# Kernel tuning notes

Measured on AMD Instinct MI355X. Metric: run time of the kernel, lower is better.

The kernel has to match this reference:

```python
import jax, jax.numpy as jnp
import numpy as np

B, T, D_IN, H = 256, 512, 64, 128
S_MIN, S_FRAC = 0.5, 0.5


def _gru_cell(x_i, h, W_ih, W_hh, b_ih, b_hh):
    # torch.nn.GRUCell semantics
    gi = x_i @ W_ih.T + b_ih          # [B, 3H]
    gh = h @ W_hh.T + b_hh            # [B, 3H]
    i_r, i_z, i_n = jnp.split(gi, 3, axis=-1)
    h_r, h_z, h_n = jnp.split(gh, 3, axis=-1)
    r = jax.nn.sigmoid(i_r + h_r)
    z = jax.nn.sigmoid(i_z + h_z)
    n = jnp.tanh(i_n + r * h_n)
    return (1.0 - z) * n + z * h


def _rk4_step(h, dt, W_node, b_node):
    # one fixed RK4 step of dh/dt = tanh(h @ W_node^T + b_node) over [t, t+dt]
    f = lambda hh: jnp.tanh(hh @ W_node.T + b_node)
    k1 = f(h)
    k2 = f(h + 0.5 * dt * k1)
    k3 = f(h + 0.5 * dt * k2)
    k4 = f(h + dt * k3)
    return h + (dt / 6.0) * (k1 + 2.0 * k2 + 2.0 * k3 + k4)


def setup_inputs() -> dict:
    key = jax.random.key(0)
    ks = jax.random.split(key, 8)
    x = jax.random.normal(ks[0], (B, T, D_IN), dtype=jnp.float32)
    # sorted per-sample time grid; all lens == T so argmax-longest picks row 0
    tp = jnp.broadcast_to(jnp.linspace(0.01, 1.0, T, dtype=jnp.float32), (B, T))
    # generate_samp_mask(x, s_min=0.5, s_frac=0.5), deterministic seed
    rng = np.random.default_rng(0)
    minimum_ind = int(T * S_MIN)
    extrap_ind = int(rng.integers(minimum_ind, T))
    n_inds = int(S_FRAC * extrap_ind)
    samp_inds = np.sort(rng.choice(np.arange(extrap_ind), n_inds, replace=False))
    mask_np = np.zeros(T, dtype=bool)
    mask_np[samp_inds] = True
    samp_mask = jnp.asarray(mask_np)
    s = 1.0 / np.sqrt(H)
    W_ih = jax.random.uniform(ks[1], (3 * H, D_IN), jnp.float32, -s, s)
    W_hh = jax.random.uniform(ks[2], (3 * H, H), jnp.float32, -s, s)
    b_ih = jax.random.uniform(ks[3], (3 * H,), jnp.float32, -s, s)
    b_hh = jax.random.uniform(ks[4], (3 * H,), jnp.float32, -s, s)
    W_node = jax.random.normal(ks[5], (H, H), jnp.float32) * 0.05
    b_node = jnp.zeros((H,), jnp.float32)
    W_out = jax.random.uniform(ks[6], (D_IN, H), jnp.float32, -s, s)
    b_out = jax.random.uniform(ks[7], (D_IN,), jnp.float32, -s, s)
    return {"x": x, "tp": tp, "samp_mask": samp_mask,
            "W_ih": W_ih, "W_hh": W_hh, "b_ih": b_ih, "b_hh": b_hh,
            "W_node": W_node, "b_node": b_node, "W_out": W_out, "b_out": b_out}


def reference(x, tp, samp_mask, W_ih, W_hh, b_ih, b_hh, W_node, b_node, W_out, b_out):
    # get_longest_tp: all lens equal -> row 0; prepend tp[0]-0.01
    t0 = tp[0]                                   # [T]
    ts = jnp.concatenate([t0[:1] - 0.01, t0])    # [T+1]
    dts = ts[1:] - ts[:-1]                       # [T]
    xs = jnp.transpose(x, (1, 0, 2))             # [T, B, D_in]
    h0 = jnp.zeros((x.shape[0], W_hh.shape[1]), x.dtype)

    def step(h, inp):
        dt, x_i, use_x = inp
        h_ode = _rk4_step(h, dt, W_node, b_node)
        prev_out = h @ W_out.T + b_out           # teacher-forcing from own output
        inp_vec = jnp.where(use_x, x_i, prev_out)
        h_new = _gru_cell(inp_vec, h_ode, W_ih, W_hh, b_ih, b_hh)
        return h_new, h_new

    _, h_arr = jax.lax.scan(step, h0, (dts, xs, samp_mask))  # [T, B, H]
    h_arr = jnp.transpose(h_arr, (1, 0, 2))                  # [B, T, H]
    out = h_arr @ W_out.T + b_out                            # [B, T, D_in]
    # select_by_length with all lens == T -> flat [B*T, D_in]
    return out.reshape(-1, out.shape[-1])
```

## Files before the change

kernel.cpp:

```cpp
#include <hip/hip_runtime.h>


#define NB    256
#define TB    512
#define TSTEP 512
#define DIN   64
#define HD    128

typedef float v2f __attribute__((ext_vector_type(2)));

__device__ __forceinline__ float fast_tanh(float v) {
    float e = __expf(2.0f * v);
    return 1.0f - 2.0f / (e + 1.0f);
}
__device__ __forceinline__ float fast_sigmoid(float v) {
    return 1.0f / (1.0f + __expf(-v));
}

__device__ __forceinline__ float quad_red(float v) {
    v += __int_as_float(__builtin_amdgcn_update_dpp(
            0, __float_as_int(v), 0xB1, 0xF, 0xF, true));
    v += __int_as_float(__builtin_amdgcn_update_dpp(
            0, __float_as_int(v), 0x4E, 0xF, 0xF, true));
    return v;
}

__global__ __launch_bounds__(TB, 2) void gruode_kernel(
    const float* __restrict__ x,
    const float* __restrict__ tp,
    const int*   __restrict__ samp_mask,
    const float* __restrict__ W_ih,
    const float* __restrict__ W_hh,
    const float* __restrict__ b_ih,
    const float* __restrict__ b_hh,
    const float* __restrict__ W_node,
    const float* __restrict__ b_node,
    const float* __restrict__ W_out,
    const float* __restrict__ b_out,
    float*       __restrict__ out)
{
    const int t   = threadIdx.x;
    const int b   = blockIdx.x;
    const int j   = t >> 2;
    const int kq  = t & 3;
    const int j64 = t >> 3;
    const int ko  = t & 7;

    __shared__ __align__(16) float sh_h [HD];
    __shared__ __align__(16) float sh_t0[HD];
    __shared__ __align__(16) float sh_t1[HD];
    __shared__ __align__(16) float sh_in[DIN];
    __shared__ __align__(16) float sh_po[DIN];

    const float4* Wn4  = (const float4*)W_node;
    const float4* Whh4 = (const float4*)W_hh;
    const float4* Wih4 = (const float4*)W_ih;
    const float4* Wo4  = (const float4*)W_out;

    v2f Wn[16], Whr[16], Whz[16], Whn[16];
    #pragma unroll
    for (int i = 0; i < 8; ++i) {
        float4 w;
        w = Wn4 [j*32 + i*4 + kq];          Wn [2*i] = (v2f){w.x, w.y}; Wn [2*i+1] = (v2f){w.z, w.w};
        w = Whh4[(0*HD + j)*32 + i*4 + kq]; Whr[2*i] = (v2f){w.x, w.y}; Whr[2*i+1] = (v2f){w.z, w.w};
        w = Whh4[(1*HD + j)*32 + i*4 + kq]; Whz[2*i] = (v2f){w.x, w.y}; Whz[2*i+1] = (v2f){w.z, w.w};
        w = Whh4[(2*HD + j)*32 + i*4 + kq]; Whn[2*i] = (v2f){w.x, w.y}; Whn[2*i+1] = (v2f){w.z, w.w};
    }
    v2f Wir[8], Wiz[8], Win[8], Wo[8];
    #pragma unroll
    for (int i = 0; i < 4; ++i) {
        float4 w;
        w = Wih4[(0*HD + j)*16 + i*4 + kq]; Wir[2*i] = (v2f){w.x, w.y}; Wir[2*i+1] = (v2f){w.z, w.w};
        w = Wih4[(1*HD + j)*16 + i*4 + kq]; Wiz[2*i] = (v2f){w.x, w.y}; Wiz[2*i+1] = (v2f){w.z, w.w};
        w = Wih4[(2*HD + j)*16 + i*4 + kq]; Win[2*i] = (v2f){w.x, w.y}; Win[2*i+1] = (v2f){w.z, w.w};
        w = Wo4 [j64*32 + i*8 + ko];        Wo [2*i] = (v2f){w.x, w.y}; Wo [2*i+1] = (v2f){w.z, w.w};
    }
    #pragma unroll
    for (int i = 0; i < 16; ++i) {
        asm volatile("" : "+v"(Wn[i]));  asm volatile("" : "+v"(Whr[i]));
        asm volatile("" : "+v"(Whz[i])); asm volatile("" : "+v"(Whn[i]));
    }
    #pragma unroll
    for (int i = 0; i < 8; ++i) {
        asm volatile("" : "+v"(Wir[i])); asm volatile("" : "+v"(Wiz[i]));
        asm volatile("" : "+v"(Win[i])); asm volatile("" : "+v"(Wo[i]));
    }

    const float bn   = b_node[j];
    const float br   = b_ih[0*HD + j] + b_hh[0*HD + j];
    const float bz   = b_ih[1*HD + j] + b_hh[1*HD + j];
    const float bi_n = b_ih[2*HD + j];
    const float bh_n = b_hh[2*HD + j];
    const float bo   = b_out[j64];

    if (t < HD)  sh_h[t]  = 0.0f;
    if (t < DIN) sh_po[t] = b_out[t];

    float tp_cur  = tp[0];
    float tp_prev = tp_cur - 0.01f;
    int   m_cur   = samp_mask[0];
    float xr = (t < DIN) ? x[(size_t)b * TSTEP * DIN + t] : 0.0f;

    __syncthreads();

    const float4* h4  = (const float4*)sh_h;
    const float4* t04 = (const float4*)sh_t0;
    const float4* t14 = (const float4*)sh_t1;
    const float4* in4 = (const float4*)sh_in;

    auto hdot = [&](const v2f (&w)[16], const float4* buf) -> float {
        v2f a0 = {0.f, 0.f}, a1 = {0.f, 0.f};
        #pragma unroll
        for (int i = 0; i < 8; ++i) {
            float4 v = buf[i*4 + kq];
            a0 += w[2*i]   * (v2f){v.x, v.y};
            a1 += w[2*i+1] * (v2f){v.z, v.w};
        }
        v2f a = a0 + a1;
        return a.x + a.y;
    };

    float hj = 0.0f;

    #pragma unroll 1
    for (int s = 0; s < TSTEP; ++s) {
        const float dt = tp_cur - tp_prev;

        if (t < DIN) sh_in[t] = m_cur ? xr : sh_po[t];

        {
            const int sn = (s + 1 < TSTEP) ? s + 1 : s;
            tp_prev = tp_cur;
            tp_cur  = tp[sn];
            m_cur   = samp_mask[sn];
            if (t < DIN) xr = x[((size_t)b * TSTEP + sn) * DIN + t];
        }

        float k1 = fast_tanh(quad_red(hdot(Wn, h4)) + bn);
        if (kq == 0) sh_t0[j] = fmaf(0.5f * dt, k1, hj);
        __syncthreads();

        float k2 = fast_tanh(quad_red(hdot(Wn, t04)) + bn);
        if (kq == 0) sh_t1[j] = fmaf(0.5f * dt, k2, hj);
        __syncthreads();

        float k3 = fast_tanh(quad_red(hdot(Wn, t14)) + bn);
        if (kq == 0) sh_t0[j] = fmaf(dt, k3, hj);
        __syncthreads();

        float k4 = fast_tanh(quad_red(hdot(Wn, t04)) + bn);
        float hode = fmaf(dt * (1.0f / 6.0f),
                          (k1 + 2.0f * k2) + (2.0f * k3 + k4), hj);
        if (kq == 0) sh_t1[j] = hode;
        __syncthreads();

        v2f ar = {0.f,0.f}, az = {0.f,0.f}, an = {0.f,0.f};
        #pragma unroll
        for (int i = 0; i < 8; ++i) {
            float4 v = t14[i*4 + kq];
            v2f lo = {v.x, v.y}, hi = {v.z, v.w};
            ar += Whr[2*i] * lo; ar += Whr[2*i+1] * hi;
            az += Whz[2*i] * lo; az += Whz[2*i+1] * hi;
            an += Whn[2*i] * lo; an += Whn[2*i+1] * hi;
        }
        v2f cr = {0.f,0.f}, cz = {0.f,0.f}, cn = {0.f,0.f};
        #pragma unroll
        for (int i = 0; i < 4; ++i) {
            float4 v = in4[i*4 + kq];
            v2f lo = {v.x, v.y}, hi = {v.z, v.w};
            cr += Wir[2*i] * lo; cr += Wir[2*i+1] * hi;
            cz += Wiz[2*i] * lo; cz += Wiz[2*i+1] * hi;
            cn += Win[2*i] * lo; cn += Win[2*i+1] * hi;
        }
        float rr  = fast_sigmoid(quad_red((ar.x + ar.y) + (cr.x + cr.y)) + br);
        float zz  = fast_sigmoid(quad_red((az.x + az.y) + (cz.x + cz.y)) + bz);
        float hnv = quad_red(an.x + an.y) + bh_n;
        float inv = quad_red(cn.x + cn.y) + bi_n;
        float nn  = fast_tanh(fmaf(rr, hnv, inv));
        float hnew = fmaf(zz, hode - nn, nn);
        hj = hnew;

        if (kq == 0) sh_h[j] = hnew;
        __syncthreads();

        v2f ao = {0.f, 0.f};
        #pragma unroll
        for (int i = 0; i < 4; ++i) {
            float4 v = h4[i*8 + ko];
            ao += Wo[2*i]   * (v2f){v.x, v.y};
            ao += Wo[2*i+1] * (v2f){v.z, v.w};
        }
        float o = quad_red(ao.x + ao.y);
        o += __shfl_xor(o, 4);
        o += bo;
        if (ko == 0) {
            sh_po[j64] = o;
            out[((size_t)b * TSTEP + s) * DIN + j64] = o;
        }
        __syncthreads();
    }
}

extern "C" void kernel_launch(void* const* d_in, const int* in_sizes, int n_in,
                              void* d_out, int out_size, void* d_ws, size_t ws_size,
                              hipStream_t stream) {
    (void)in_sizes; (void)n_in; (void)d_ws; (void)ws_size; (void)out_size;
    const float* x      = (const float*)d_in[0];
    const float* tp     = (const float*)d_in[1];
    const int*   mask   = (const int*)  d_in[2];
    const float* W_ih   = (const float*)d_in[3];
    const float* W_hh   = (const float*)d_in[4];
    const float* b_ih   = (const float*)d_in[5];
    const float* b_hh   = (const float*)d_in[6];
    const float* W_node = (const float*)d_in[7];
    const float* b_node = (const float*)d_in[8];
    const float* W_out  = (const float*)d_in[9];
    const float* b_out  = (const float*)d_in[10];
    float* outp = (float*)d_out;

    gruode_kernel<<<NB, TB, 0, stream>>>(x, tp, mask, W_ih, W_hh, b_ih, b_hh,
                                         W_node, b_node, W_out, b_out, outp);
}
```

Baseline: 1.225 ms.

## Remap to 16-lane groups computing 4 rows each with DPP scan reductions

Each thread now owns a 16-wide slice of the K dimension for four output rows, rather than a quarter of one row. Per-row sums are reduced across the 16 lanes with row_shr DPP scans, and the total is broadcast with a quad_perm so each of the last four lanes picks up one row. The GRU input vector is now read directly from registers (x) or sh_po, which removes the sh_in staging buffer and one barrier per timestep, and x is loaded as float4. Fewer barriers and wider loads are traded for more DPP instructions per reduction and a select at the end of every dot product.

```diff
diff --git a/kernel.cpp b/kernel.cpp
--- a/kernel.cpp
+++ b/kernel.cpp
@@ -17,15 +17,25 @@
     return 1.0f / (1.0f + __expf(-v));
 }
 
-__device__ __forceinline__ float quad_red(float v) {
-    v += __int_as_float(__builtin_amdgcn_update_dpp(
-            0, __float_as_int(v), 0xB1, 0xF, 0xF, true));
-    v += __int_as_float(__builtin_amdgcn_update_dpp(
-            0, __float_as_int(v), 0x4E, 0xF, 0xF, true));
+template<int CTRL>
+__device__ __forceinline__ float dpp_add(float v) {
+    return v + __int_as_float(__builtin_amdgcn_update_dpp(
+        0, __float_as_int(v), CTRL, 0xF, 0xF, true));
+}
+__device__ __forceinline__ float scan16(float v) {
+    v = dpp_add<0x111>(v);
+    v = dpp_add<0x112>(v);
+    v = dpp_add<0x114>(v);
+    v = dpp_add<0x118>(v);
     return v;
 }
-
-__global__ __launch_bounds__(TB, 2) void gruode_kernel(
+__device__ __forceinline__ float qp3333(float v) {
+    return __int_as_float(__builtin_amdgcn_update_dpp(
+        0, __float_as_int(v), 0xFF, 0xF, 0xF, true));
+}
+
+__global__ __launch_bounds__(TB) __attribute__((amdgpu_waves_per_eu(2, 2)))
+void gruode_kernel(
     const float* __restrict__ x,
     const float* __restrict__ tp,
     const int*   __restrict__ samp_mask,
@@ -39,17 +49,15 @@
     const float* __restrict__ b_out,
     float*       __restrict__ out)
 {
-    const int t   = threadIdx.x;
-    const int b   = blockIdx.x;
-    const int j   = t >> 2;
-    const int kq  = t & 3;
-    const int j64 = t >> 3;
-    const int ko  = t & 7;
+    const int t    = threadIdx.x;
+    const int b    = blockIdx.x;
+    const int g    = t >> 4;
+    const int kk   = t & 15;
+    const int rsel = kk & 3;
 
     __shared__ __align__(16) float sh_h [HD];
     __shared__ __align__(16) float sh_t0[HD];
     __shared__ __align__(16) float sh_t1[HD];
-    __shared__ __align__(16) float sh_in[DIN];
     __shared__ __align__(16) float sh_po[DIN];
 
     const float4* Wn4  = (const float4*)W_node;
@@ -57,41 +65,57 @@
     const float4* Wih4 = (const float4*)W_ih;
     const float4* Wo4  = (const float4*)W_out;
 
-    v2f Wn[16], Whr[16], Whz[16], Whn[16];
-    #pragma unroll
-    for (int i = 0; i < 8; ++i) {
-        float4 w;
-        w = Wn4 [j*32 + i*4 + kq];          Wn [2*i] = (v2f){w.x, w.y}; Wn [2*i+1] = (v2f){w.z, w.w};
-        w = Whh4[(0*HD + j)*32 + i*4 + kq]; Whr[2*i] = (v2f){w.x, w.y}; Whr[2*i+1] = (v2f){w.z, w.w};
-        w = Whh4[(1*HD + j)*32 + i*4 + kq]; Whz[2*i] = (v2f){w.x, w.y}; Whz[2*i+1] = (v2f){w.z, w.w};
-        w = Whh4[(2*HD + j)*32 + i*4 + kq]; Whn[2*i] = (v2f){w.x, w.y}; Whn[2*i+1] = (v2f){w.z, w.w};
-    }
-    v2f Wir[8], Wiz[8], Win[8], Wo[8];
+    v2f Wn[4][4], Whr[4][4], Whz[4][4], Whn[4][4];
+    v2f Wir[4][2], Wiz[4][2], Win[4][2];
+    v2f Wo[2][4];
+    #pragma unroll
+    for (int r = 0; r < 4; ++r) {
+        const int row = 4*g + r;
+        float4 a, c;
+        a = Wn4[row*32 + 2*kk];  c = Wn4[row*32 + 2*kk + 1];
+        Wn[r][0]=(v2f){a.x,a.y}; Wn[r][1]=(v2f){a.z,a.w}; Wn[r][2]=(v2f){c.x,c.y}; Wn[r][3]=(v2f){c.z,c.w};
+        a = Whh4[(0*HD+row)*32 + 2*kk];  c = Whh4[(0*HD+row)*32 + 2*kk + 1];
+        Whr[r][0]=(v2f){a.x,a.y}; Whr[r][1]=(v2f){a.z,a.w}; Whr[r][2]=(v2f){c.x,c.y}; Whr[r][3]=(v2f){c.z,c.w};
+        a = Whh4[(1*HD+row)*32 + 2*kk];  c = Whh4[(1*HD+row)*32 + 2*kk + 1];
+        Whz[r][0]=(v2f){a.x,a.y}; Whz[r][1]=(v2f){a.z,a.w}; Whz[r][2]=(v2f){c.x,c.y}; Whz[r][3]=(v2f){c.z,c.w};
+        a = Whh4[(2*HD+row)*32 + 2*kk];  c = Whh4[(2*HD+row)*32 + 2*kk + 1];
+        Whn[r][0]=(v2f){a.x,a.y}; Whn[r][1]=(v2f){a.z,a.w}; Whn[r][2]=(v2f){c.x,c.y}; Whn[r][3]=(v2f){c.z,c.w};
+        a = Wih4[(0*HD+row)*16 + kk];
+        Wir[r][0]=(v2f){a.x,a.y}; Wir[r][1]=(v2f){a.z,a.w};
+        a = Wih4[(1*HD+row)*16 + kk];
+        Wiz[r][0]=(v2f){a.x,a.y}; Wiz[r][1]=(v2f){a.z,a.w};
+        a = Wih4[(2*HD+row)*16 + kk];
+        Win[r][0]=(v2f){a.x,a.y}; Win[r][1]=(v2f){a.z,a.w};
+    }
+    #pragma unroll
+    for (int r = 0; r < 2; ++r) {
+        const int row = 2*g + r;
+        float4 a = Wo4[row*32 + 2*kk], c = Wo4[row*32 + 2*kk + 1];
+        Wo[r][0]=(v2f){a.x,a.y}; Wo[r][1]=(v2f){a.z,a.w}; Wo[r][2]=(v2f){c.x,c.y}; Wo[r][3]=(v2f){c.z,c.w};
+    }
+    #pragma unroll
+    for (int r = 0; r < 4; ++r) {
+        #pragma unroll
+        for (int i = 0; i < 4; ++i) {
+            asm volatile("" : "+v"(Wn[r][i]));  asm volatile("" : "+v"(Whr[r][i]));
+            asm volatile("" : "+v"(Whz[r][i])); asm volatile("" : "+v"(Whn[r][i]));
+        }
+        asm volatile("" : "+v"(Wir[r][0])); asm volatile("" : "+v"(Wir[r][1]));
+        asm volatile("" : "+v"(Wiz[r][0])); asm volatile("" : "+v"(Wiz[r][1]));
+        asm volatile("" : "+v"(Win[r][0])); asm volatile("" : "+v"(Win[r][1]));
+    }
     #pragma unroll
     for (int i = 0; i < 4; ++i) {
-        float4 w;
-        w = Wih4[(0*HD + j)*16 + i*4 + kq]; Wir[2*i] = (v2f){w.x, w.y}; Wir[2*i+1] = (v2f){w.z, w.w};
-        w = Wih4[(1*HD + j)*16 + i*4 + kq]; Wiz[2*i] = (v2f){w.x, w.y}; Wiz[2*i+1] = (v2f){w.z, w.w};
-        w = Wih4[(2*HD + j)*16 + i*4 + kq]; Win[2*i] = (v2f){w.x, w.y}; Win[2*i+1] = (v2f){w.z, w.w};
-        w = Wo4 [j64*32 + i*8 + ko];        Wo [2*i] = (v2f){w.x, w.y}; Wo [2*i+1] = (v2f){w.z, w.w};
-    }
-    #pragma unroll
-    for (int i = 0; i < 16; ++i) {
-        asm volatile("" : "+v"(Wn[i]));  asm volatile("" : "+v"(Whr[i]));
-        asm volatile("" : "+v"(Whz[i])); asm volatile("" : "+v"(Whn[i]));
-    }
-    #pragma unroll
-    for (int i = 0; i < 8; ++i) {
-        asm volatile("" : "+v"(Wir[i])); asm volatile("" : "+v"(Wiz[i]));
-        asm volatile("" : "+v"(Win[i])); asm volatile("" : "+v"(Wo[i]));
-    }
-
-    const float bn   = b_node[j];
-    const float br   = b_ih[0*HD + j] + b_hh[0*HD + j];
-    const float bz   = b_ih[1*HD + j] + b_hh[1*HD + j];
-    const float bi_n = b_ih[2*HD + j];
-    const float bh_n = b_hh[2*HD + j];
-    const float bo   = b_out[j64];
+        asm volatile("" : "+v"(Wo[0][i])); asm volatile("" : "+v"(Wo[1][i]));
+    }
+
+    const int rl  = 4*g + rsel;
+    const float bn   = b_node[rl];
+    const float br   = b_ih[0*HD + rl] + b_hh[0*HD + rl];
+    const float bz   = b_ih[1*HD + rl] + b_hh[1*HD + rl];
+    const float bin  = b_ih[2*HD + rl];
+    const float bhn  = b_hh[2*HD + rl];
+    const float bo   = b_out[2*g + (rsel & 1)];
 
     if (t < HD)  sh_h[t]  = 0.0f;
     if (t < DIN) sh_po[t] = b_out[t];
@@ -99,25 +123,34 @@
     float tp_cur  = tp[0];
     float tp_prev = tp_cur - 0.01f;
     int   m_cur   = samp_mask[0];
-    float xr = (t < DIN) ? x[(size_t)b * TSTEP * DIN + t] : 0.0f;
+    const float4* x4 = (const float4*)x;
+    float4 xr = x4[(size_t)b * TSTEP * 16 + kk];
 
     __syncthreads();
 
     const float4* h4  = (const float4*)sh_h;
     const float4* t04 = (const float4*)sh_t0;
     const float4* t14 = (const float4*)sh_t1;
-    const float4* in4 = (const float4*)sh_in;
-
-    auto hdot = [&](const v2f (&w)[16], const float4* buf) -> float {
-        v2f a0 = {0.f, 0.f}, a1 = {0.f, 0.f};
+    const float4* po4 = (const float4*)sh_po;
+
+    auto dot128 = [&](const v2f (&w)[4][4], const float4* buf, float (&acc)[4]) {
+        float4 a = buf[2*kk], c = buf[2*kk + 1];
+        v2f x0 = {a.x, a.y}, x1 = {a.z, a.w}, x2 = {c.x, c.y}, x3 = {c.z, c.w};
         #pragma unroll
-        for (int i = 0; i < 8; ++i) {
-            float4 v = buf[i*4 + kq];
-            a0 += w[2*i]   * (v2f){v.x, v.y};
-            a1 += w[2*i+1] * (v2f){v.z, v.w};
-        }
-        v2f a = a0 + a1;
-        return a.x + a.y;
+        for (int r = 0; r < 4; ++r) {
+            v2f s = w[r][0] * x0;
+            s = w[r][1] * x1 + s;
+            s = w[r][2] * x2 + s;
+            s = w[r][3] * x3 + s;
+            acc[r] = s.x + s.y;
+        }
+    };
+    auto reduce4 = [&](const float (&acc)[4]) -> float {
+        float s0 = qp3333(scan16(acc[0]));
+        float s1 = qp3333(scan16(acc[1]));
+        float s2 = qp3333(scan16(acc[2]));
+        float s3 = qp3333(scan16(acc[3]));
+        return rsel == 0 ? s0 : rsel == 1 ? s1 : rsel == 2 ? s2 : s3;
     };
 
     float hj = 0.0f;
@@ -125,79 +158,99 @@
     #pragma unroll 1
     for (int s = 0; s < TSTEP; ++s) {
         const float dt = tp_cur - tp_prev;
-
-        if (t < DIN) sh_in[t] = m_cur ? xr : sh_po[t];
+        float acc[4], p, k1, k2, k3, k4;
+
+        dot128(Wn, h4, acc);
+        p  = reduce4(acc);
+        k1 = fast_tanh(p + bn);
+        if (kk >= 12) sh_t0[4*g + rsel] = fmaf(0.5f * dt, k1, hj);
+        __syncthreads();
+
+        dot128(Wn, t04, acc);
+        p  = reduce4(acc);
+        k2 = fast_tanh(p + bn);
+        if (kk >= 12) sh_t1[4*g + rsel] = fmaf(0.5f * dt, k2, hj);
+        __syncthreads();
+
+        dot128(Wn, t14, acc);
+        p  = reduce4(acc);
+        k3 = fast_tanh(p + bn);
+        if (kk >= 12) sh_t0[4*g + rsel] = fmaf(dt, k3, hj);
+        __syncthreads();
+
+        dot128(Wn, t04, acc);
+        p  = reduce4(acc);
+        k4 = fast_tanh(p + bn);
+        const float hode = fmaf(dt * (1.0f / 6.0f),
+                                (k1 + 2.0f * k2) + (2.0f * k3 + k4), hj);
+        if (kk >= 12) sh_t1[4*g + rsel] = hode;
+        __syncthreads();
+
+        {
+            float4 a = t14[2*kk], c = t14[2*kk + 1];
+            v2f h0 = {a.x, a.y}, h1 = {a.z, a.w}, h2 = {c.x, c.y}, h3 = {c.z, c.w};
+            float4 vi;
+            if (m_cur) vi = xr; else vi = po4[kk];
+            v2f i0 = {vi.x, vi.y}, i1 = {vi.z, vi.w};
+
+            float aR[4], aZ[4], aNh[4], aNi[4];
+            #pragma unroll
+            for (int r = 0; r < 4; ++r) {
+                v2f sR = Whr[r][0]*h0; sR = Whr[r][1]*h1 + sR;
+                sR = Whr[r][2]*h2 + sR; sR = Whr[r][3]*h3 + sR;
+                sR = Wir[r][0]*i0 + sR; sR = Wir[r][1]*i1 + sR;
+                aR[r] = sR.x + sR.y;
+                v2f sZ = Whz[r][0]*h0; sZ = Whz[r][1]*h1 + sZ;
+                sZ = Whz[r][2]*h2 + sZ; sZ = Whz[r][3]*h3 + sZ;
+                sZ = Wiz[r][0]*i0 + sZ; sZ = Wiz[r][1]*i1 + sZ;
+                aZ[r] = sZ.x + sZ.y;
+                v2f sH = Whn[r][0]*h0; sH = Whn[r][1]*h1 + sH;
+                sH = Whn[r][2]*h2 + sH; sH = Whn[r][3]*h3 + sH;
+                aNh[r] = sH.x + sH.y;
+                v2f sI = Win[r][0]*i0; sI = Win[r][1]*i1 + sI;
+                aNi[r] = sI.x + sI.y;
+            }
+            float R  = reduce4(aR);
+            float Z  = reduce4(aZ);
+            float Nh = reduce4(aNh);
+            float Ni = reduce4(aNi);
+
+            float rr = fast_sigmoid(R + br);
+            float zz = fast_sigmoid(Z + bz);
+            float nn = fast_tanh(fmaf(rr, Nh + bhn, Ni + bin));
+            float hnew = fmaf(zz, hode - nn, nn);
+            hj = hnew;
+            if (kk >= 12) sh_h[4*g + rsel] = hnew;
+        }
 
         {
             const int sn = (s + 1 < TSTEP) ? s + 1 : s;
             tp_prev = tp_cur;
             tp_cur  = tp[sn];
             m_cur   = samp_mask[sn];
-            if (t < DIN) xr = x[((size_t)b * TSTEP + sn) * DIN + t];
-        }
-
-        float k1 = fast_tanh(quad_red(hdot(Wn, h4)) + bn);
-        if (kq == 0) sh_t0[j] = fmaf(0.5f * dt, k1, hj);
-        __syncthreads();
-
-        float k2 = fast_tanh(quad_red(hdot(Wn, t04)) + bn);
-        if (kq == 0) sh_t1[j] = fmaf(0.5f * dt, k2, hj);
-        __syncthreads();
-
-        float k3 = fast_tanh(quad_red(hdot(Wn, t14)) + bn);
-        if (kq == 0) sh_t0[j] = fmaf(dt, k3, hj);
-        __syncthreads();
-
-        float k4 = fast_tanh(quad_red(hdot(Wn, t04)) + bn);
-        float hode = fmaf(dt * (1.0f / 6.0f),
-                          (k1 + 2.0f * k2) + (2.0f * k3 + k4), hj);
-        if (kq == 0) sh_t1[j] = hode;
-        __syncthreads();
-
-        v2f ar = {0.f,0.f}, az = {0.f,0.f}, an = {0.f,0.f};
-        #pragma unroll
-        for (int i = 0; i < 8; ++i) {
-            float4 v = t14[i*4 + kq];
-            v2f lo = {v.x, v.y}, hi = {v.z, v.w};
-            ar += Whr[2*i] * lo; ar += Whr[2*i+1] * hi;
-            az += Whz[2*i] * lo; az += Whz[2*i+1] * hi;
-            an += Whn[2*i] * lo; an += Whn[2*i+1] * hi;
-        }
-        v2f cr = {0.f,0.f}, cz = {0.f,0.f}, cn = {0.f,0.f};
-        #pragma unroll
-        for (int i = 0; i < 4; ++i) {
-            float4 v = in4[i*4 + kq];
-            v2f lo = {v.x, v.y}, hi = {v.z, v.w};
-            cr += Wir[2*i] * lo; cr += Wir[2*i+1] * hi;
-            cz += Wiz[2*i] * lo; cz += Wiz[2*i+1] * hi;
-            cn += Win[2*i] * lo; cn += Win[2*i+1] * hi;
-        }
-        float rr  = fast_sigmoid(quad_red((ar.x + ar.y) + (cr.x + cr.y)) + br);
-        float zz  = fast_sigmoid(quad_red((az.x + az.y) + (cz.x + cz.y)) + bz);
-        float hnv = quad_red(an.x + an.y) + bh_n;
-        float inv = quad_red(cn.x + cn.y) + bi_n;
-        float nn  = fast_tanh(fmaf(rr, hnv, inv));
-        float hnew = fmaf(zz, hode - nn, nn);
-        hj = hnew;
-
-        if (kq == 0) sh_h[j] = hnew;
-        __syncthreads();
-
-        v2f ao = {0.f, 0.f};
-        #pragma unroll
-        for (int i = 0; i < 4; ++i) {
-            float4 v = h4[i*8 + ko];
-            ao += Wo[2*i]   * (v2f){v.x, v.y};
-            ao += Wo[2*i+1] * (v2f){v.z, v.w};
-        }
-        float o = quad_red(ao.x + ao.y);
-        o += __shfl_xor(o, 4);
-        o += bo;
-        if (ko == 0) {
-            sh_po[j64] = o;
-            out[((size_t)b * TSTEP + s) * DIN + j64] = o;
-        }
-        __syncthreads();
+            xr = x4[((size_t)b * TSTEP + sn) * 16 + kk];
+        }
+        __syncthreads();
+
+        {
+            float4 a = h4[2*kk], c = h4[2*kk + 1];
+            v2f x0 = {a.x, a.y}, x1 = {a.z, a.w}, x2 = {c.x, c.y}, x3 = {c.z, c.w};
+            float o01[2];
+            #pragma unroll
+            for (int r = 0; r < 2; ++r) {
+                v2f s2_ = Wo[r][0]*x0; s2_ = Wo[r][1]*x1 + s2_;
+                s2_ = Wo[r][2]*x2 + s2_; s2_ = Wo[r][3]*x3 + s2_;
+                o01[r] = s2_.x + s2_.y;
+            }
+            float so0 = qp3333(scan16(o01[0]));
+            float so1 = qp3333(scan16(o01[1]));
+            float o = ((rsel & 1) ? so1 : so0) + bo;
+            if (kk == 12 || kk == 13) {
+                const int col = 2*g + rsel;
+                sh_po[col] = o;
+                out[((size_t)b * TSTEP + s) * DIN + col] = o;
+            }
+        }
     }
 }
 
```

New measurement: 1.411 ms. 15.2% more time.

## Split each hidden unit across 8 lanes with 1024-thread blocks and padded LDS

Applied to the files above, without the earlier changes.

The block grows from 512 to 1024 threads, so each hidden unit gets 8 lanes instead of 4 and each lane holds half as many weight registers. Lane partial sums are combined with a three-step DPP row-shift scan, with the result read by the last lane of each group. The hidden-state buffers use a padded stride to avoid LDS bank conflicts, and x inputs are double-buffered in shared memory. W_out moves from registers into padded shared memory. Shorter per-lane dot products are meant to cut the latency of each serial step, at the cost of more threads per barrier and an extra LDS read stream for the output projection.

```diff
diff --git a/kernel.cpp b/kernel.cpp
--- a/kernel.cpp
+++ b/kernel.cpp
@@ -2,11 +2,15 @@
 
 
 #define NB    256
-#define TB    512
+#define TB    1024
 #define TSTEP 512
 #define DIN   64
 #define HD    128
 
+#define HSTRIDE 20
+#define HSZ     160
+#define WOSTRIDE 164
+
 typedef float v2f __attribute__((ext_vector_type(2)));
 
 __device__ __forceinline__ float fast_tanh(float v) {
@@ -17,15 +21,20 @@
     return 1.0f / (1.0f + __expf(-v));
 }
 
-__device__ __forceinline__ float quad_red(float v) {
-    v += __int_as_float(__builtin_amdgcn_update_dpp(
-            0, __float_as_int(v), 0xB1, 0xF, 0xF, true));
-    v += __int_as_float(__builtin_amdgcn_update_dpp(
-            0, __float_as_int(v), 0x4E, 0xF, 0xF, true));
+template<int CTRL>
+__device__ __forceinline__ float dpp_add(float v) {
+    return v + __int_as_float(__builtin_amdgcn_update_dpp(
+        0, __float_as_int(v), CTRL, 0xF, 0xF, true));
+}
+__device__ __forceinline__ float scan8(float v) {
+    v = dpp_add<0x111>(v);
+    v = dpp_add<0x112>(v);
+    v = dpp_add<0x114>(v);
     return v;
 }
 
-__global__ __launch_bounds__(TB, 2) void gruode_kernel(
+__global__ __launch_bounds__(TB) __attribute__((amdgpu_waves_per_eu(4, 4)))
+void gruode_kernel(
     const float* __restrict__ x,
     const float* __restrict__ tp,
     const int*   __restrict__ samp_mask,
@@ -39,163 +48,188 @@
     const float* __restrict__ b_out,
     float*       __restrict__ out)
 {
-    const int t   = threadIdx.x;
-    const int b   = blockIdx.x;
-    const int j   = t >> 2;
-    const int kq  = t & 3;
-    const int j64 = t >> 3;
-    const int ko  = t & 7;
-
-    __shared__ __align__(16) float sh_h [HD];
-    __shared__ __align__(16) float sh_t0[HD];
-    __shared__ __align__(16) float sh_t1[HD];
-    __shared__ __align__(16) float sh_in[DIN];
+    const int t     = threadIdx.x;
+    const int b     = blockIdx.x;
+    const int g     = t >> 3;
+    const int kkk   = t & 7;
+    const bool owner = (kkk == 7);
+    const int gsw   = HSTRIDE * (g >> 4) + (g & 15);
+
+    __shared__ __align__(16) float sh_h [HSZ];
+    __shared__ __align__(16) float sh_t0[HSZ];
+    __shared__ __align__(16) float sh_t1[HSZ];
+    __shared__ __align__(16) float sh_x [2][DIN];
     __shared__ __align__(16) float sh_po[DIN];
+    __shared__ __align__(16) float sh_wout[DIN * WOSTRIDE];
 
     const float4* Wn4  = (const float4*)W_node;
     const float4* Whh4 = (const float4*)W_hh;
     const float4* Wih4 = (const float4*)W_ih;
     const float4* Wo4  = (const float4*)W_out;
 
-    v2f Wn[16], Whr[16], Whz[16], Whn[16];
+    v2f Wn[8], Whr[8], Whz[8], Whn[8];
+    #pragma unroll
+    for (int u = 0; u < 4; ++u) {
+        float4 w;
+        w = Wn4[g*32 + kkk*4 + u];
+        Wn [2*u] = (v2f){w.x, w.y}; Wn [2*u+1] = (v2f){w.z, w.w};
+        w = Whh4[(0*HD + g)*32 + kkk*4 + u];
+        Whr[2*u] = (v2f){w.x, w.y}; Whr[2*u+1] = (v2f){w.z, w.w};
+        w = Whh4[(1*HD + g)*32 + kkk*4 + u];
+        Whz[2*u] = (v2f){w.x, w.y}; Whz[2*u+1] = (v2f){w.z, w.w};
+        w = Whh4[(2*HD + g)*32 + kkk*4 + u];
+        Whn[2*u] = (v2f){w.x, w.y}; Whn[2*u+1] = (v2f){w.z, w.w};
+    }
+    v2f Wir[4], Wiz[4], Win[4];
+    #pragma unroll
+    for (int u = 0; u < 2; ++u) {
+        float4 w;
+        w = Wih4[(0*HD + g)*16 + kkk*2 + u];
+        Wir[2*u] = (v2f){w.x, w.y}; Wir[2*u+1] = (v2f){w.z, w.w};
+        w = Wih4[(1*HD + g)*16 + kkk*2 + u];
+        Wiz[2*u] = (v2f){w.x, w.y}; Wiz[2*u+1] = (v2f){w.z, w.w};
+        w = Wih4[(2*HD + g)*16 + kkk*2 + u];
+        Win[2*u] = (v2f){w.x, w.y}; Win[2*u+1] = (v2f){w.z, w.w};
+    }
     #pragma unroll
     for (int i = 0; i < 8; ++i) {
-        float4 w;
-        w = Wn4 [j*32 + i*4 + kq];          Wn [2*i] = (v2f){w.x, w.y}; Wn [2*i+1] = (v2f){w.z, w.w};
-        w = Whh4[(0*HD + j)*32 + i*4 + kq]; Whr[2*i] = (v2f){w.x, w.y}; Whr[2*i+1] = (v2f){w.z, w.w};
-        w = Whh4[(1*HD + j)*32 + i*4 + kq]; Whz[2*i] = (v2f){w.x, w.y}; Whz[2*i+1] = (v2f){w.z, w.w};
-        w = Whh4[(2*HD + j)*32 + i*4 + kq]; Whn[2*i] = (v2f){w.x, w.y}; Whn[2*i+1] = (v2f){w.z, w.w};
-    }
-    v2f Wir[8], Wiz[8], Win[8], Wo[8];
-    #pragma unroll
-    for (int i = 0; i < 4; ++i) {
-        float4 w;
-        w = Wih4[(0*HD + j)*16 + i*4 + kq]; Wir[2*i] = (v2f){w.x, w.y}; Wir[2*i+1] = (v2f){w.z, w.w};
-        w = Wih4[(1*HD + j)*16 + i*4 + kq]; Wiz[2*i] = (v2f){w.x, w.y}; Wiz[2*i+1] = (v2f){w.z, w.w};
-        w = Wih4[(2*HD + j)*16 + i*4 + kq]; Win[2*i] = (v2f){w.x, w.y}; Win[2*i+1] = (v2f){w.z, w.w};
-        w = Wo4 [j64*32 + i*8 + ko];        Wo [2*i] = (v2f){w.x, w.y}; Wo [2*i+1] = (v2f){w.z, w.w};
-    }
-    #pragma unroll
-    for (int i = 0; i < 16; ++i) {
         asm volatile("" : "+v"(Wn[i]));  asm volatile("" : "+v"(Whr[i]));
         asm volatile("" : "+v"(Whz[i])); asm volatile("" : "+v"(Whn[i]));
     }
     #pragma unroll
-    for (int i = 0; i < 8; ++i) {
+    for (int i = 0; i < 4; ++i) {
         asm volatile("" : "+v"(Wir[i])); asm volatile("" : "+v"(Wiz[i]));
-        asm volatile("" : "+v"(Win[i])); asm volatile("" : "+v"(Wo[i]));
-    }
-
-    const float bn   = b_node[j];
-    const float br   = b_ih[0*HD + j] + b_hh[0*HD + j];
-    const float bz   = b_ih[1*HD + j] + b_hh[1*HD + j];
-    const float bi_n = b_ih[2*HD + j];
-    const float bh_n = b_hh[2*HD + j];
-    const float bo   = b_out[j64];
-
-    if (t < HD)  sh_h[t]  = 0.0f;
+        asm volatile("" : "+v"(Win[i]));
+    }
+
+    const float bn  = b_node[g];
+    const float br  = b_ih[0*HD + g] + b_hh[0*HD + g];
+    const float bz  = b_ih[1*HD + g] + b_hh[1*HD + g];
+    const float bin = b_ih[2*HD + g];
+    const float bhn = b_hh[2*HD + g];
+    const float bo  = (g < DIN) ? b_out[g] : 0.0f;
+
+    if (t < HD)  sh_h[HSTRIDE*(t>>4) + (t&15)] = 0.0f;
     if (t < DIN) sh_po[t] = b_out[t];
-
-    float tp_cur  = tp[0];
-    float tp_prev = tp_cur - 0.01f;
-    int   m_cur   = samp_mask[0];
-    float xr = (t < DIN) ? x[(size_t)b * TSTEP * DIN + t] : 0.0f;
-
+    if (t < DIN) sh_x[0][t] = x[(size_t)b * TSTEP * DIN + t];
+    if (t < 512) {
+        const int gg = t >> 3, k2 = t & 7;
+        #pragma unroll
+        for (int u = 0; u < 4; ++u) {
+            float4 w = Wo4[gg*32 + k2*4 + u];
+            *(float4*)(sh_wout + gg*WOSTRIDE + k2*HSTRIDE + 4*u) = w;
+        }
+    }
     __syncthreads();
 
-    const float4* h4  = (const float4*)sh_h;
-    const float4* t04 = (const float4*)sh_t0;
-    const float4* t14 = (const float4*)sh_t1;
-    const float4* in4 = (const float4*)sh_in;
-
-    auto hdot = [&](const v2f (&w)[16], const float4* buf) -> float {
+    const int bufoff = HSTRIDE * kkk;
+
+    auto dot16 = [&](const v2f (&w)[8], const float* buf) -> float {
+        const float4* p = (const float4*)(buf + bufoff);
         v2f a0 = {0.f, 0.f}, a1 = {0.f, 0.f};
         #pragma unroll
-        for (int i = 0; i < 8; ++i) {
-            float4 v = buf[i*4 + kq];
-            a0 += w[2*i]   * (v2f){v.x, v.y};
-            a1 += w[2*i+1] * (v2f){v.z, v.w};
+        for (int u = 0; u < 4; ++u) {
+            float4 v = p[u];
+            a0 = w[2*u]   * (v2f){v.x, v.y} + a0;
+            a1 = w[2*u+1] * (v2f){v.z, v.w} + a1;
         }
         v2f a = a0 + a1;
         return a.x + a.y;
     };
 
     float hj = 0.0f;
+    float tp_prev = tp[0] - 0.01f;
 
     #pragma unroll 1
     for (int s = 0; s < TSTEP; ++s) {
-        const float dt = tp_cur - tp_prev;
-
-        if (t < DIN) sh_in[t] = m_cur ? xr : sh_po[t];
+        const float tpv   = tp[s];
+        const int   m_cur = samp_mask[s];
+        const float dt    = tpv - tp_prev;
+        tp_prev = tpv;
+
+        const int sn = (s + 1 < TSTEP) ? s + 1 : s;
+        float xn = 0.0f;
+        if (t < DIN) xn = x[((size_t)b * TSTEP + sn) * DIN + t];
+
+        float k1 = fast_tanh(scan8(dot16(Wn, sh_h)) + bn);
+        if (owner) sh_t0[gsw] = fmaf(0.5f*dt, k1, hj);
+        __syncthreads();
+
+        float k2 = fast_tanh(scan8(dot16(Wn, sh_t0)) + bn);
+        if (owner) sh_t1[gsw] = fmaf(0.5f*dt, k2, hj);
+        __syncthreads();
+
+        float k3 = fast_tanh(scan8(dot16(Wn, sh_t1)) + bn);
+        if (owner) sh_t0[gsw] = fmaf(dt, k3, hj);
+        __syncthreads();
+
+        float k4 = fast_tanh(scan8(dot16(Wn, sh_t0)) + bn);
+        const float hode = fmaf(dt * (1.0f/6.0f),
+                                (k1 + 2.0f*k2) + (2.0f*k3 + k4), hj);
+        if (owner) sh_t1[gsw] = hode;
+        if (t < DIN) sh_x[(s + 1) & 1][t] = xn;
+        __syncthreads();
 
         {
-            const int sn = (s + 1 < TSTEP) ? s + 1 : s;
-            tp_prev = tp_cur;
-            tp_cur  = tp[sn];
-            m_cur   = samp_mask[sn];
-            if (t < DIN) xr = x[((size_t)b * TSTEP + sn) * DIN + t];
-        }
-
-        float k1 = fast_tanh(quad_red(hdot(Wn, h4)) + bn);
-        if (kq == 0) sh_t0[j] = fmaf(0.5f * dt, k1, hj);
-        __syncthreads();
-
-        float k2 = fast_tanh(quad_red(hdot(Wn, t04)) + bn);
-        if (kq == 0) sh_t1[j] = fmaf(0.5f * dt, k2, hj);
-        __syncthreads();
-
-        float k3 = fast_tanh(quad_red(hdot(Wn, t14)) + bn);
-        if (kq == 0) sh_t0[j] = fmaf(dt, k3, hj);
-        __syncthreads();
-
-        float k4 = fast_tanh(quad_red(hdot(Wn, t04)) + bn);
-        float hode = fmaf(dt * (1.0f / 6.0f),
-                          (k1 + 2.0f * k2) + (2.0f * k3 + k4), hj);
-        if (kq == 0) sh_t1[j] = hode;
-        __syncthreads();
-
-        v2f ar = {0.f,0.f}, az = {0.f,0.f}, an = {0.f,0.f};
-        #pragma unroll
-        for (int i = 0; i < 8; ++i) {
-            float4 v = t14[i*4 + kq];
-            v2f lo = {v.x, v.y}, hi = {v.z, v.w};
-            ar += Whr[2*i] * lo; ar += Whr[2*i+1] * hi;
-            az += Whz[2*i] * lo; az += Whz[2*i+1] * hi;
-            an += Whn[2*i] * lo; an += Whn[2*i+1] * hi;
-        }
-        v2f cr = {0.f,0.f}, cz = {0.f,0.f}, cn = {0.f,0.f};
-        #pragma unroll
-        for (int i = 0; i < 4; ++i) {
-            float4 v = in4[i*4 + kq];
-            v2f lo = {v.x, v.y}, hi = {v.z, v.w};
-            cr += Wir[2*i] * lo; cr += Wir[2*i+1] * hi;
-            cz += Wiz[2*i] * lo; cz += Wiz[2*i+1] * hi;
-            cn += Win[2*i] * lo; cn += Win[2*i+1] * hi;
-        }
-        float rr  = fast_sigmoid(quad_red((ar.x + ar.y) + (cr.x + cr.y)) + br);
-        float zz  = fast_sigmoid(quad_red((az.x + az.y) + (cz.x + cz.y)) + bz);
-        float hnv = quad_red(an.x + an.y) + bh_n;
-        float inv = quad_red(cn.x + cn.y) + bi_n;
-        float nn  = fast_tanh(fmaf(rr, hnv, inv));
-        float hnew = fmaf(zz, hode - nn, nn);
-        hj = hnew;
-
-        if (kq == 0) sh_h[j] = hnew;
-        __syncthreads();
-
-        v2f ao = {0.f, 0.f};
-        #pragma unroll
-        for (int i = 0; i < 4; ++i) {
-            float4 v = h4[i*8 + ko];
-            ao += Wo[2*i]   * (v2f){v.x, v.y};
-            ao += Wo[2*i+1] * (v2f){v.z, v.w};
-        }
-        float o = quad_red(ao.x + ao.y);
-        o += __shfl_xor(o, 4);
-        o += bo;
-        if (ko == 0) {
-            sh_po[j64] = o;
-            out[((size_t)b * TSTEP + s) * DIN + j64] = o;
+            const float* insrc = m_cur ? sh_x[s & 1] : sh_po;
+            const float4* pi = (const float4*)(insrc + 8*kkk);
+            const float4* ph = (const float4*)(sh_t1 + bufoff);
+
+            v2f sR = {0.f,0.f}, sZ = {0.f,0.f}, sH = {0.f,0.f}, sI = {0.f,0.f};
+            {
+                float4 va = ph[0], vb = ph[1];
+                v2f h0={va.x,va.y}, h1={va.z,va.w}, h2={vb.x,vb.y}, h3={vb.z,vb.w};
+                sR = Whr[0]*h0+sR; sR = Whr[1]*h1+sR; sR = Whr[2]*h2+sR; sR = Whr[3]*h3+sR;
+                sZ = Whz[0]*h0+sZ; sZ = Whz[1]*h1+sZ; sZ = Whz[2]*h2+sZ; sZ = Whz[3]*h3+sZ;
+                sH = Whn[0]*h0+sH; sH = Whn[1]*h1+sH; sH = Whn[2]*h2+sH; sH = Whn[3]*h3+sH;
+            }
+            {
+                float4 vc = ph[2], vd = ph[3];
+                v2f h4={vc.x,vc.y}, h5={vc.z,vc.w}, h6={vd.x,vd.y}, h7={vd.z,vd.w};
+                sR = Whr[4]*h4+sR; sR = Whr[5]*h5+sR; sR = Whr[6]*h6+sR; sR = Whr[7]*h7+sR;
+                sZ = Whz[4]*h4+sZ; sZ = Whz[5]*h5+sZ; sZ = Whz[6]*h6+sZ; sZ = Whz[7]*h7+sZ;
+                sH = Whn[4]*h4+sH; sH = Whn[5]*h5+sH; sH = Whn[6]*h6+sH; sH = Whn[7]*h7+sH;
+            }
+            {
+                float4 w0 = pi[0], w1 = pi[1];
+                v2f i0={w0.x,w0.y}, i1={w0.z,w0.w}, i2={w1.x,w1.y}, i3={w1.z,w1.w};
+                sR = Wir[0]*i0+sR; sR = Wir[1]*i1+sR; sR = Wir[2]*i2+sR; sR = Wir[3]*i3+sR;
+                sZ = Wiz[0]*i0+sZ; sZ = Wiz[1]*i1+sZ; sZ = Wiz[2]*i2+sZ; sZ = Wiz[3]*i3+sZ;
+                sI = Win[0]*i0+sI; sI = Win[1]*i1+sI; sI = Win[2]*i2+sI; sI = Win[3]*i3+sI;
+            }
+
+            float R  = scan8(sR.x + sR.y);
+            float Z  = scan8(sZ.x + sZ.y);
+            float Nh = scan8(sH.x + sH.y);
+            float Ni = scan8(sI.x + sI.y);
+
+            float rr = fast_sigmoid(R + br);
+            float zz = fast_sigmoid(Z + bz);
+            float nn = fast_tanh(fmaf(rr, Nh + bhn, Ni + bin));
+            float hnew = fmaf(zz, hode - nn, nn);
+            hj = hnew;
+            if (owner) sh_h[gsw] = hnew;
+        }
+        __syncthreads();
+
+        if (g < DIN) {
+            const float4* pw = (const float4*)(sh_wout + g*WOSTRIDE + bufoff);
+            const float4* ph = (const float4*)(sh_h + bufoff);
+            v2f a0 = {0.f,0.f}, a1 = {0.f,0.f};
+            #pragma unroll
+            for (int u = 0; u < 4; ++u) {
+                float4 wv = pw[u];
+                float4 hv = ph[u];
+                a0 = (v2f){wv.x,wv.y} * (v2f){hv.x,hv.y} + a0;
+                a1 = (v2f){wv.z,wv.w} * (v2f){hv.z,hv.w} + a1;
+            }
+            v2f a = a0 + a1;
+            float o = scan8(a.x + a.y);
+            if (owner) {
+                float oo = o + bo;
+                sh_po[g] = oo;
+                out[((size_t)b * TSTEP + s) * DIN + g] = oo;
+            }
         }
         __syncthreads();
     }
```

Measured after the change: 1.901 ms. 1.55x slower.
